# Kernel tuning notes

Hardware: AMD Instinct MI355X
Metric: run time of the kernel (lower is better)

The kernel has to match this reference:

```python
import jax, jax.numpy as jnp
import numpy as np

# Single LSTM cell step from ZERO initial state (h0=c0=0), vectorized over (B,T).
# PyTorch gate order: i, f, g, o. Since h0=0 the W_hh contribution is exactly 0
# and since c0=0 the forget-gate term vanishes: c = sigmoid(i)*tanh(g).

def _cell(inp, W_ih, b_ih, b_hh):
    # inp: (B,T,in), W_ih: (4H,in) -> gates (B,T,4H)
    g = jnp.einsum('bti,gi->btg', inp, W_ih) + b_ih + b_hh
    i_, f_, g_, o_ = jnp.split(g, 4, axis=-1)
    c = jax.nn.sigmoid(i_) * jnp.tanh(g_)
    h = jax.nn.sigmoid(o_) * jnp.tanh(c)
    return h, c


def setup_inputs() -> dict:
    key = jax.random.key(0)
    ks = jax.random.split(key, 11)
    B, T, E, H, V = 32, 256, 512, 512, 50000
    s = 1.0 / np.sqrt(H)  # keep gates out of deep saturation
    return {
        'x': jax.random.randint(ks[0], (B, T), 0, V, dtype=jnp.int32),
        'emb': jax.random.normal(ks[1], (V, E), jnp.float32),
        'W_ih_l0': jax.random.normal(ks[2], (2, 4 * H, E), jnp.float32) * s,
        'W_hh_l0': jax.random.normal(ks[3], (2, 4 * H, H), jnp.float32) * s,
        'b_ih_l0': jax.random.normal(ks[4], (2, 4 * H), jnp.float32) * s,
        'b_hh_l0': jax.random.normal(ks[5], (2, 4 * H), jnp.float32) * s,
        'W_ih_l1': jax.random.normal(ks[6], (2, 4 * H, 2 * H), jnp.float32) * s,
        'W_hh_l1': jax.random.normal(ks[7], (2, 4 * H, H), jnp.float32) * s,
        'b_ih_l1': jax.random.normal(ks[8], (2, 4 * H), jnp.float32) * s,
        'b_hh_l1': jax.random.normal(ks[9], (2, 4 * H), jnp.float32) * s,
    }


def reference(x, emb, W_ih_l0, W_hh_l0, b_ih_l0, b_hh_l0,
              W_ih_l1, W_hh_l1, b_ih_l1, b_hh_l1):
    e = emb[x]  # (B,T,E)
    # layer 0, forward/backward directions (seq_len==1 per step, so both
    # directions see the same token from zero state, with separate weights)
    h0f, c0f = _cell(e, W_ih_l0[0], b_ih_l0[0], b_hh_l0[0])
    h0b, c0b = _cell(e, W_ih_l0[1], b_ih_l0[1], b_hh_l0[1])
    inp1 = jnp.concatenate([h0f, h0b], axis=-1)  # (B,T,2H)
    h1f, c1f = _cell(inp1, W_ih_l1[0], b_ih_l1[0], b_hh_l1[0])
    h1b, c1b = _cell(inp1, W_ih_l1[1], b_ih_l1[1], b_hh_l1[1])
    # encoder_out: per-timestep h_n summed over directions -> (B,T,L,H)
    encoder_out = jnp.stack([h0f + h0b, h1f + h1b], axis=2)
    # h_last: forward-direction h_n and c_n at last timestep -> (L,B,H)
    h_last = jnp.stack([h0f[:, -1], h1f[:, -1]], axis=0)
    c_last = jnp.stack([c0f[:, -1], c1f[:, -1]], axis=0)
    return h_last, c_last, encoder_out
```

## Files before the change

### kernel.cpp

```cpp
#include <hip/hip_runtime.h>
#include <hip/hip_bf16.h>


using bf16x8 = __attribute__((ext_vector_type(8))) short;
using f32x4  = __attribute__((ext_vector_type(4))) float;

__device__ __forceinline__ unsigned short f2bf(float f)
{
    __hip_bfloat16 h = __float2bfloat16(f);
    return *(unsigned short*)&h;
}
__device__ __forceinline__ float sigf(float x)  { return 1.0f / (1.0f + __expf(-x)); }
__device__ __forceinline__ float tanhfast(float x)
{
    return 1.0f - 2.0f / (__expf(2.0f * x) + 1.0f);
}

__device__ __forceinline__ void gload16(const void* g, void* l)
{
    __builtin_amdgcn_global_load_lds(
        (const __attribute__((address_space(1))) unsigned int*)g,
        (__attribute__((address_space(3))) unsigned int*)l, 16, 0, 0);
}
#define SBAR() do { __builtin_amdgcn_sched_barrier(0); \
                    __builtin_amdgcn_s_barrier();      \
                    __builtin_amdgcn_sched_barrier(0); } while (0)

__global__ __launch_bounds__(256)
void prep(const int* __restrict__ x, const void* __restrict__ emb,
          const void* __restrict__ Wih0, const void* __restrict__ Wih1,
          const void* __restrict__ bih0, const void* __restrict__ bhh0,
          const void* __restrict__ bih1, const void* __restrict__ bhh1,
          uint4* __restrict__ e0, uint4* __restrict__ Wp0, uint4* __restrict__ Wp1,
          float* __restrict__ bc0, float* __restrict__ bc1, int* __restrict__ flag)
{
    __shared__ int oks[4];
    __shared__ uint4 panel[32][65];
    {
        unsigned lo = ((const unsigned int*)emb)[threadIdx.x] & 0xFFFFu;
        int e = (lo >> 7) & 0xFF;
        int ok = ((e >= 96 && e < 160) || lo == 0) ? 1 : 0;
#pragma unroll
        for (int off = 32; off; off >>= 1) ok += __shfl_down(ok, off);
        if ((threadIdx.x & 63) == 0) oks[threadIdx.x >> 6] = ok;
    }
    __syncthreads();
    const bool isbf = (oks[0] + oks[1] + oks[2] + oks[3]) >= 192;
    const int bid = blockIdx.x, tid = threadIdx.x;

    if (bid < 256) {
        const int mbase = bid * 32;
#pragma unroll
        for (int j = 0; j < 8; ++j) {
            int li = j * 256 + tid;
            int ml = li >> 6, k8 = li & 63;
            long srow = x[mbase + ml];
            uint4 v;
            if (isbf) {
                v = ((const uint4*)emb)[srow * 64 + k8];
            } else {
                const float4* ef = (const float4*)emb;
                float4 a = ef[srow * 128 + k8 * 2], b = ef[srow * 128 + k8 * 2 + 1];
                unsigned short h[8] = { f2bf(a.x), f2bf(a.y), f2bf(a.z), f2bf(a.w),
                                        f2bf(b.x), f2bf(b.y), f2bf(b.z), f2bf(b.w) };
                v = *(uint4*)h;
            }
            panel[ml][k8] = v;
        }
        __syncthreads();
#pragma unroll
        for (int j = 0; j < 8; ++j) {
            int li = j * 256 + tid;
            int k8 = li >> 5, ml = li & 31;
            e0[(long)k8 * 8192 + mbase + ml] = panel[ml][k8];
        }
    } else if (bid < 544) {
        const bool L0 = bid < 352;
        const int t = L0 ? (bid - 256) : (bid - 352);
        const int nbase  = (L0 ? t : (t >> 1)) * 32;
        const int k8base = L0 ? 0 : (t & 1) * 64;
        const void* src = L0 ? Wih0 : Wih1;
        uint4* dst = L0 ? Wp0 : Wp1;
        const int K8s = L0 ? 64 : 128;
#pragma unroll
        for (int j = 0; j < 8; ++j) {
            int li = j * 256 + tid;
            int nl = li >> 6, k8l = li & 63;
            int n = nbase + nl;
            int h = n / 6, gi = n - h * 6;
            int dir = (gi >= 3) ? 1 : 0;
            int gate = gi - dir * 3;
            int sg = (gate == 0) ? 0 : (gate + 1);
            long srcrow = dir * 2048 + sg * 512 + h;
            uint4 v;
            if (isbf) {
                v = ((const uint4*)src)[srcrow * K8s + k8base + k8l];
            } else {
                const float4* sf = (const float4*)src;
                long c2 = (srcrow * K8s + k8base + k8l) * 2;
                float4 a = sf[c2], b = sf[c2 + 1];
                unsigned short h8[8] = { f2bf(a.x), f2bf(a.y), f2bf(a.z), f2bf(a.w),
                                         f2bf(b.x), f2bf(b.y), f2bf(b.z), f2bf(b.w) };
                v = *(uint4*)h8;
            }
            panel[nl][k8l] = v;
        }
        __syncthreads();
#pragma unroll
        for (int j = 0; j < 8; ++j) {
            int li = j * 256 + tid;
            int k8l = li >> 5, nl = li & 31;
            dst[(long)(k8base + k8l) * 3072 + nbase + nl] = panel[nl][k8l];
        }
    } else {
        int b2 = bid - 544;
        if (b2 == 0 && tid == 0) *flag = isbf ? 1 : 0;
        const bool L0 = b2 < 12;
        int n = (L0 ? b2 : (b2 - 12)) * 256 + tid;
        int h = n / 6, gi = n - h * 6;
        int dir = (gi >= 3) ? 1 : 0;
        int gate = gi - dir * 3;
        int sg = (gate == 0) ? 0 : (gate + 1);
        int s = dir * 2048 + sg * 512 + h;
        const void* bi = L0 ? bih0 : bih1;
        const void* bh = L0 ? bhh0 : bhh1;
        float* bc = L0 ? bc0 : bc1;
        float vi, vh;
        if (isbf) {
            vi = __bfloat162float(((const __hip_bfloat16*)bi)[s]);
            vh = __bfloat162float(((const __hip_bfloat16*)bh)[s]);
        } else {
            vi = ((const float*)bi)[s];
            vh = ((const float*)bh)[s];
        }
        bc[n] = vi + vh;
    }
}

template <int LAYER, int K>
__global__ __launch_bounds__(512)
void gemm_fused(const unsigned short* __restrict__ A,
                const unsigned short* __restrict__ Bp,
                const float* __restrict__ bc,
                unsigned short* __restrict__ inp1,
                void* __restrict__ outv,
                const int* __restrict__ flag)
{
    constexpr int NT = K / 32;
    __shared__ __align__(16) char smem[67584];

    const int tid = threadIdx.x;
    const int raw = blockIdx.x + (blockIdx.y << 5);
    const int xcd = raw & 7, local = raw >> 3;
    const int bm = xcd * 4 + (local >> 5);
    const int bn = local & 31;

    const uint4* a4 = (const uint4*)A;
    const uint4* b4 = (const uint4*)Bp;

    const int btid = (tid < 384) ? tid : (tid - 128);
    const long aOff = (long)(tid >> 8) * 8192 + bm * 256 + (tid & 255);
    const long bOff = (long)(btid / 96) * 3072 + bn * 96 + (btid % 96);

    const int wave = tid >> 6, lane = tid & 63;
    const int wr = (wave >> 1) * 64;
    const int wc = (wave & 1) * 48;
    const int lr = lane & 15, q = lane >> 4;

    f32x4 acc[4][3] = {};

    auto stage = [&](int s) {
        const int buf = s % 3;
        uint4* As4 = (uint4*)(smem + buf * 16384);
        uint4* Bs4 = (uint4*)(smem + 49152 + buf * 6144);
        const uint4* ap = a4 + (long)s * 32768 + aOff;
        gload16(ap, As4 + tid);
        gload16(ap + 16384, As4 + tid + 512);
        gload16(b4 + (long)s * 12288 + bOff, Bs4 + btid);
    };

    stage(0);
    stage(1);
#pragma unroll
    for (int t = 0; t < NT; ++t) {
        if (t + 2 < NT) {
            stage(t + 2);
            asm volatile("s_waitcnt vmcnt(6)" ::: "memory");
        } else if (t + 1 < NT) {
            asm volatile("s_waitcnt vmcnt(3)" ::: "memory");
        } else {
            asm volatile("s_waitcnt vmcnt(0)" ::: "memory");
        }
        SBAR();

        const unsigned short* As = (const unsigned short*)(smem + (t % 3) * 16384);
        const unsigned short* Bs = (const unsigned short*)(smem + 49152 + (t % 3) * 6144);
        bf16x8 af[4], bf[3];
#pragma unroll
        for (int i = 0; i < 4; ++i)
            af[i] = *(const bf16x8*)&As[(q * 256 + wr + i * 16 + lr) * 8];
#pragma unroll
        for (int j = 0; j < 3; ++j)
            bf[j] = *(const bf16x8*)&Bs[(q * 96 + wc + j * 16 + lr) * 8];
        __builtin_amdgcn_s_setprio(1);
#pragma unroll
        for (int i = 0; i < 4; ++i)
#pragma unroll
            for (int j = 0; j < 3; ++j)
                acc[i][j] = __builtin_amdgcn_mfma_f32_16x16x32_bf16(af[i], bf[j], acc[i][j], 0, 0, 0);
        __builtin_amdgcn_s_setprio(0);
        SBAR();
    }

    float* Cs = (float*)smem;
    const bool isbf = (*flag != 0);
    auto store = [&](long i, float v) {
        if (isbf) ((__hip_bfloat16*)outv)[i] = __float2bfloat16(v);
        else      ((float*)outv)[i] = v;
    };

    const int hl = tid & 15;
    float bcv[6];
#pragma unroll
    for (int gi = 0; gi < 6; ++gi) bcv[gi] = bc[bn * 96 + hl * 6 + gi];

    for (int p = 0; p < 4; ++p) {
        if ((wave >> 1) == p) {
#pragma unroll
            for (int i = 0; i < 4; ++i)
#pragma unroll
                for (int j = 0; j < 3; ++j)
#pragma unroll
                    for (int r = 0; r < 4; ++r)
                        Cs[(i * 16 + q * 4 + r) * 97 + wc + j * 16 + lr] = acc[i][j][r];
        }
        __syncthreads();
#pragma unroll
        for (int t2 = 0; t2 < 2; ++t2) {
            int ml = (tid >> 4) + t2 * 32;
            float z[6];
#pragma unroll
            for (int gi = 0; gi < 6; ++gi) z[gi] = Cs[ml * 97 + hl * 6 + gi] + bcv[gi];
            float c0 = sigf(z[0]) * tanhfast(z[1]);
            float h0 = sigf(z[2]) * tanhfast(c0);
            float c1 = sigf(z[3]) * tanhfast(z[4]);
            float h1 = sigf(z[5]) * tanhfast(c1);

            long m = (long)bm * 256 + p * 64 + ml;
            int hg = bn * 16 + hl;

            if constexpr (LAYER == 0) {
                int c0i = hg, c1i = 512 + hg;
                inp1[((long)(c0i >> 3) * 8192 + m) * 8 + (c0i & 7)] = f2bf(h0);
                inp1[((long)(c1i >> 3) * 8192 + m) * 8 + (c1i & 7)] = f2bf(h1);
            }
            store(65536 + m * 1024 + LAYER * 512 + hg, h0 + h1);
            if ((m & 255) == 255) {
                int b = (int)(m >> 8);
                store(LAYER * 16384 + b * 512 + hg, h0);
                store(32768 + LAYER * 16384 + b * 512 + hg, c0);
            }
        }
        if (p < 3) __syncthreads();
    }
}

extern "C" void kernel_launch(void* const* d_in, const int* in_sizes, int n_in,
                              void* d_out, int out_size, void* d_ws, size_t ws_size,
                              hipStream_t stream)
{
    const int* x      = (const int*)d_in[0];
    const void* emb   = d_in[1];
    const void* Wih0  = d_in[2];
    const void* bih0  = d_in[4];
    const void* bhh0  = d_in[5];
    const void* Wih1  = d_in[6];
    const void* bih1  = d_in[8];
    const void* bhh1  = d_in[9];

    char* ws = (char*)d_ws;
    int*   flag           = (int*)(ws);
    float* bc0            = (float*)(ws + 1024);
    float* bc1            = (float*)(ws + 16384);
    unsigned short* Wp0   = (unsigned short*)(ws + 32768);
    unsigned short* Wp1   = (unsigned short*)(ws + 4194304);
    unsigned short* e0    = (unsigned short*)(ws + 10485760);
    unsigned short* inp1  = (unsigned short*)(ws + 18874368);

    prep<<<568, 256, 0, stream>>>(x, emb, Wih0, Wih1, bih0, bhh0, bih1, bhh1,
                                  (uint4*)e0, (uint4*)Wp0, (uint4*)Wp1, bc0, bc1, flag);

    gemm_fused<0, 512><<<dim3(32, 32), 512, 0, stream>>>(e0, Wp0, bc0, inp1, d_out, flag);
    gemm_fused<1, 1024><<<dim3(32, 32), 512, 0, stream>>>(inp1, Wp1, bc1, nullptr, d_out, flag);
}
```

Measured before the change: 287.6 us.

## Use K=64 tiles with double buffering instead of K=32 triple buffering

Each pipeline stage now covers 64 elements of K instead of 32, so there are half as many iterations and barriers, and each iteration issues 24 MFMAs per wave. The LDS pipeline drops from three buffers to two, with a re-laid-out shared memory of 90 KB. Prefetch depth in K stays about the same, but the exposed latency per stage may grow, and the larger LDS footprint may limit how many blocks fit on a CU.

```diff
diff --git a/kernel.cpp b/kernel.cpp
--- a/kernel.cpp
+++ b/kernel.cpp
@@ -146,8 +146,8 @@
                 void* __restrict__ outv,
                 const int* __restrict__ flag)
 {
-    constexpr int NT = K / 32;
-    __shared__ __align__(16) char smem[67584];
+    constexpr int NT = K / 64;
+    __shared__ __align__(16) char smem[90112];
 
     const int tid = threadIdx.x;
     const int raw = blockIdx.x + (blockIdx.y << 5);
@@ -170,44 +170,50 @@
     f32x4 acc[4][3] = {};
 
     auto stage = [&](int s) {
-        const int buf = s % 3;
-        uint4* As4 = (uint4*)(smem + buf * 16384);
-        uint4* Bs4 = (uint4*)(smem + 49152 + buf * 6144);
-        const uint4* ap = a4 + (long)s * 32768 + aOff;
-        gload16(ap, As4 + tid);
-        gload16(ap + 16384, As4 + tid + 512);
-        gload16(b4 + (long)s * 12288 + bOff, Bs4 + btid);
+        const int buf = s & 1;
+        uint4* As4 = (uint4*)(smem + 24576 + buf * 32768);
+        uint4* Bs4 = (uint4*)(smem + buf * 12288);
+        const uint4* ap = a4 + (long)s * 65536 + aOff;
+        gload16(ap,          As4 + tid);
+        gload16(ap + 16384,  As4 + tid + 512);
+        gload16(ap + 32768,  As4 + tid + 1024);
+        gload16(ap + 49152,  As4 + tid + 1536);
+        const uint4* bp = b4 + (long)s * 24576 + bOff;
+        gload16(bp,          Bs4 + btid);
+        gload16(bp + 12288,  Bs4 + btid + 384);
     };
 
     stage(0);
-    stage(1);
 #pragma unroll
     for (int t = 0; t < NT; ++t) {
-        if (t + 2 < NT) {
-            stage(t + 2);
+        if (t + 1 < NT) {
+            stage(t + 1);
             asm volatile("s_waitcnt vmcnt(6)" ::: "memory");
-        } else if (t + 1 < NT) {
-            asm volatile("s_waitcnt vmcnt(3)" ::: "memory");
         } else {
             asm volatile("s_waitcnt vmcnt(0)" ::: "memory");
         }
         SBAR();
 
-        const unsigned short* As = (const unsigned short*)(smem + (t % 3) * 16384);
-        const unsigned short* Bs = (const unsigned short*)(smem + 49152 + (t % 3) * 6144);
-        bf16x8 af[4], bf[3];
-#pragma unroll
-        for (int i = 0; i < 4; ++i)
-            af[i] = *(const bf16x8*)&As[(q * 256 + wr + i * 16 + lr) * 8];
-#pragma unroll
-        for (int j = 0; j < 3; ++j)
-            bf[j] = *(const bf16x8*)&Bs[(q * 96 + wc + j * 16 + lr) * 8];
+        const unsigned short* As = (const unsigned short*)(smem + 24576 + (t & 1) * 32768);
+        const unsigned short* Bs = (const unsigned short*)(smem + (t & 1) * 12288);
+        bf16x8 af[2][4], bfr[2][3];
+#pragma unroll
+        for (int s = 0; s < 2; ++s) {
+#pragma unroll
+            for (int i = 0; i < 4; ++i)
+                af[s][i] = *(const bf16x8*)&As[((s * 4 + q) * 256 + wr + i * 16 + lr) * 8];
+#pragma unroll
+            for (int j = 0; j < 3; ++j)
+                bfr[s][j] = *(const bf16x8*)&Bs[((s * 4 + q) * 96 + wc + j * 16 + lr) * 8];
+        }
         __builtin_amdgcn_s_setprio(1);
 #pragma unroll
-        for (int i = 0; i < 4; ++i)
-#pragma unroll
-            for (int j = 0; j < 3; ++j)
-                acc[i][j] = __builtin_amdgcn_mfma_f32_16x16x32_bf16(af[i], bf[j], acc[i][j], 0, 0, 0);
+        for (int s = 0; s < 2; ++s)
+#pragma unroll
+            for (int i = 0; i < 4; ++i)
+#pragma unroll
+                for (int j = 0; j < 3; ++j)
+                    acc[i][j] = __builtin_amdgcn_mfma_f32_16x16x32_bf16(af[s][i], bfr[s][j], acc[i][j], 0, 0, 0);
         __builtin_amdgcn_s_setprio(0);
         SBAR();
     }
```

After: 312.2 us. 8.6% more time.
